# Kernel optimization log

Measured on AMD Instinct MI355X. Metric: run time of the kernel, lower is better.

The kernel has to match this reference:

```python
import jax, jax.numpy as jnp
import numpy as np

D = 256
N_EDGES = 8192
N_CORNERS = 4096


def setup_inputs() -> dict:
    key = jax.random.key(0)
    ks = jax.random.split(key, 8)
    scale = 1.0 / np.sqrt(D)
    return {
        "edge_pred": jax.random.uniform(ks[0], (N_EDGES,), dtype=jnp.float32),
        "edge_corner": jax.random.randint(ks[1], (N_EDGES, 2), 0, N_CORNERS, dtype=jnp.int64),
        "all_corners": jax.random.uniform(ks[2], (N_CORNERS, 2), dtype=jnp.float32),
        "edge_x": jax.random.normal(ks[3], (N_EDGES, D), dtype=jnp.float32),
        "image_x": jax.random.normal(ks[4], (1024,), dtype=jnp.float32),
        "W1": jax.random.normal(ks[5], (D, D), dtype=jnp.float32) * scale,
        "b1": jnp.zeros((D,), dtype=jnp.float32),
        "W2": jax.random.normal(ks[6], (D, D), dtype=jnp.float32) * scale,
        "b2": jnp.zeros((D,), dtype=jnp.float32),
        "W3": jax.random.normal(ks[7], (3 * D, D), dtype=jnp.float32) * scale,
        "b3": jnp.zeros((D,), dtype=jnp.float32),
    }


def _linear_block(x, W, b):
    # LinearBlock: Linear followed by ReLU
    return jax.nn.relu(x @ W + b)


def reference(edge_pred, edge_corner, all_corners, edge_x, image_x, W1, b1, W2, b2, W3, b3):
    # 'fully' branch of MPModule.forward. edge_pred/edge_corner/all_corners/image_x
    # are unused in this branch (kept for signature fidelity).
    e1 = _linear_block(edge_x, W1, b1)              # [N, D]
    # (e1.unsqueeze(1) * e1).mean(-1) == (e1 @ e1.T) / D   -> [N, N]
    sim1 = (e1 @ e1.T) / D
    e2 = _linear_block(edge_x, W2, b2)
    sim2 = (e2 @ e2.T) / D
    # (edge_x * sim.unsqueeze(-1)).sum(1) == sim @ edge_x  -> [N, D]
    agg1 = sim1 @ edge_x
    agg2 = sim2 @ edge_x
    cat = jnp.concatenate([edge_x, agg1, agg2], axis=-1)  # [N, 3D]
    out = _linear_block(cat, W3, b3)                      # [N, D]
    return out
```

## Files before the change

kernel.cpp:

```cpp
#include <hip/hip_runtime.h>

#define NE 8192
#define DD 256
#define NSPLIT 32

typedef __attribute__((ext_vector_type(8))) short short8;
typedef __attribute__((ext_vector_type(4))) short short4v;
typedef __attribute__((ext_vector_type(8))) __bf16 bf16x8;
typedef __attribute__((ext_vector_type(4))) float floatx4;

__device__ __forceinline__ unsigned short f2bf(float f) {
  union { float f; unsigned int i; } v; v.f = f;
  unsigned int r = v.i + 0x7fffu + ((v.i >> 16) & 1u);
  return (unsigned short)(r >> 16);
}

__device__ __forceinline__ floatx4 mfma_bf16(short8 a, short8 b, floatx4 c) {
  return __builtin_amdgcn_mfma_f32_16x16x32_bf16(
      __builtin_bit_cast(bf16x8, a), __builtin_bit_cast(bf16x8, b), c, 0, 0, 0);
}

__device__ __forceinline__ void tcvt_tile(const float* __restrict__ src, int C,
                                          unsigned short* __restrict__ dst, int R,
                                          int r0, int c0, int tid) {
  __shared__ float ls[64][68];
  const int rr = tid >> 4;
  const int c4 = (tid & 15) * 4;
#pragma unroll
  for (int k = 0; k < 4; ++k) {
    floatx4 v = *(const floatx4*)&src[(size_t)(r0 + rr + k * 16) * C + c0 + c4];
    *(floatx4*)&ls[rr + k * 16][c4] = v;
  }
  __syncthreads();
  const int cc = tid >> 2;
  const int rb = (tid & 3) * 16;
  short8 o0, o1;
#pragma unroll
  for (int i = 0; i < 8; ++i) {
    o0[i] = (short)f2bf(ls[rb + i][cc]);
    o1[i] = (short)f2bf(ls[rb + 8 + i][cc]);
  }
  unsigned short* dp = &dst[(size_t)(c0 + cc) * R + r0 + rb];
  *(short8*)dp = o0;
  *(short8*)(dp + 8) = o1;
}

__global__ void cvt_all(const float* __restrict__ x, unsigned short* __restrict__ xb,
                        unsigned short* __restrict__ xT,
                        const float* __restrict__ W1, unsigned short* __restrict__ W1t,
                        const float* __restrict__ W2, unsigned short* __restrict__ W2t,
                        const float* __restrict__ W3, unsigned short* __restrict__ W3t0) {
  const int b = blockIdx.x;
  const int tid = threadIdx.x;
  if (b < 1024) {
    int i = b * 256 + tid;
    floatx4 a = ((const floatx4*)x)[2 * i];
    floatx4 c = ((const floatx4*)x)[2 * i + 1];
    short8 o;
#pragma unroll
    for (int k = 0; k < 4; ++k) { o[k] = (short)f2bf(a[k]); o[4 + k] = (short)f2bf(c[k]); }
    ((short8*)xb)[i] = o;
  } else if (b < 1536) {
    int t = b - 1024;
    tcvt_tile(x, DD, xT, NE, (t >> 2) * 64, (t & 3) * 64, tid);
  } else if (b < 1552) {
    int t = b - 1536;
    tcvt_tile(W1, DD, W1t, DD, (t >> 2) * 64, (t & 3) * 64, tid);
  } else if (b < 1568) {
    int t = b - 1552;
    tcvt_tile(W2, DD, W2t, DD, (t >> 2) * 64, (t & 3) * 64, tid);
  } else {
    int t = b - 1568;
    tcvt_tile(W3, DD, W3t0, DD, (t >> 2) * 64, (t & 3) * 64, tid);
  }
}

template <bool F32OUT, bool STORE_T>
__global__ __launch_bounds__(256, 2)
void gemm_bias_relu(const unsigned short* __restrict__ A0, const unsigned short* __restrict__ B0,
                    const unsigned short* __restrict__ A1, const unsigned short* __restrict__ B1,
                    const unsigned short* __restrict__ A2, const unsigned short* __restrict__ B2,
                    int nseg, const float* __restrict__ bias, void* __restrict__ outp,
                    unsigned short* __restrict__ outT,
                    const unsigned short* __restrict__ B0alt, const float* __restrict__ biasalt,
                    void* __restrict__ outalt, unsigned short* __restrict__ outTalt)
{
  __shared__ unsigned short lds_a[128 * 40];
  __shared__ unsigned short lds_b[128 * 40];

  const unsigned short* B0s = B0;
  const float* bi = bias;
  void* op = outp;
  unsigned short* ot = outT;
  if (blockIdx.z) { B0s = B0alt; bi = biasalt; op = outalt; ot = outTalt; }

  const int tid  = threadIdx.x;
  const int lane = tid & 63;
  const int wave = tid >> 6;
  const int q = lane >> 4, r = lane & 15;
  const int wr = (wave >> 1) * 64;
  const int wc = (wave & 1) * 64;
  const int row0 = blockIdx.y * 128;
  const int col0 = blockIdx.x * 128;

  floatx4 acc[4][4];
#pragma unroll
  for (int i = 0; i < 4; ++i)
#pragma unroll
    for (int j = 0; j < 4; ++j) acc[i][j] = (floatx4){0.f, 0.f, 0.f, 0.f};

  const int sr = tid >> 1;
  const int sk = (tid & 1) * 16;

  for (int s = 0; s < nseg; ++s) {
    const unsigned short* A = (s == 0) ? A0 : ((s == 1) ? A1 : A2);
    const unsigned short* B = (s == 0) ? B0s : ((s == 1) ? B1 : B2);
    for (int kc = 0; kc < 256; kc += 32) {
      const unsigned short* ga = A + (size_t)(row0 + sr) * DD + kc + sk;
      short8 av0 = *(const short8*)ga;
      short8 av1 = *(const short8*)(ga + 8);
      const unsigned short* gb = B + (size_t)(col0 + sr) * DD + kc + sk;
      short8 bv0 = *(const short8*)gb;
      short8 bv1 = *(const short8*)(gb + 8);

      *(short8*)&lds_a[sr * 40 + sk]     = av0;
      *(short8*)&lds_a[sr * 40 + sk + 8] = av1;
      *(short8*)&lds_b[sr * 40 + sk]     = bv0;
      *(short8*)&lds_b[sr * 40 + sk + 8] = bv1;
      __syncthreads();

      short8 af[4], bfr[4];
#pragma unroll
      for (int i = 0; i < 4; ++i)
        af[i] = *(const short8*)&lds_a[(wr + i * 16 + r) * 40 + q * 8];
#pragma unroll
      for (int j = 0; j < 4; ++j)
        bfr[j] = *(const short8*)&lds_b[(wc + j * 16 + r) * 40 + q * 8];
#pragma unroll
      for (int i = 0; i < 4; ++i)
#pragma unroll
        for (int j = 0; j < 4; ++j)
          acc[i][j] = mfma_bf16(af[i], bfr[j], acc[i][j]);
      __syncthreads();
    }
  }

#pragma unroll
  for (int j = 0; j < 4; ++j) {
    const int col = col0 + wc + j * 16 + r;
    const float bv = bi[col];
#pragma unroll
    for (int i = 0; i < 4; ++i) {
      const int rowb = row0 + wr + i * 16 + q * 4;
      float v[4];
#pragma unroll
      for (int t = 0; t < 4; ++t) v[t] = fmaxf(acc[i][j][t] + bv, 0.0f);
      if (F32OUT) {
#pragma unroll
        for (int t = 0; t < 4; ++t)
          ((float*)op)[(size_t)(rowb + t) * DD + col] = v[t];
      } else {
#pragma unroll
        for (int t = 0; t < 4; ++t)
          ((unsigned short*)op)[(size_t)(rowb + t) * DD + col] = f2bf(v[t]);
      }
      if (STORE_T) {
        short4v tv;
#pragma unroll
        for (int t = 0; t < 4; ++t) tv[t] = (short)f2bf(v[t]);
        *(short4v*)&ot[(size_t)col * NE + rowb] = tv;
      }
    }
  }
}

__global__ __launch_bounds__(256, 2)
void atb_partial(const unsigned short* __restrict__ e1T,
                 const unsigned short* __restrict__ e2T,
                 const unsigned short* __restrict__ xT,
                 float* __restrict__ P_T)
{
  __shared__ unsigned short lds_e[128 * 40];
  __shared__ unsigned short lds_x[128 * 40];

  const int tid  = threadIdx.x;
  const int lane = tid & 63;
  const int wave = tid >> 6;
  const int q = lane >> 4, r = lane & 15;
  const int wr = (wave >> 1) * 64, wc = (wave & 1) * 64;
  const int m0 = (blockIdx.x >> 1) * 128;
  const int n0 = (blockIdx.x & 1) * 128;
  const int j0 = blockIdx.y * (NE / NSPLIT);
  const unsigned short* E = blockIdx.z ? e2T : e1T;
  float* P = P_T + (size_t)(blockIdx.z * NSPLIT + blockIdx.y) * 65536;

  floatx4 acc[4][4];
#pragma unroll
  for (int i = 0; i < 4; ++i)
#pragma unroll
    for (int j = 0; j < 4; ++j) acc[i][j] = (floatx4){0.f, 0.f, 0.f, 0.f};

  const int sr = tid >> 1;
  const int sk = (tid & 1) * 16;

  for (int jc = 0; jc < NE / NSPLIT; jc += 32) {
    const unsigned short* ge = E + (size_t)(m0 + sr) * NE + j0 + jc + sk;
    short8 ev0 = *(const short8*)ge;
    short8 ev1 = *(const short8*)(ge + 8);
    const unsigned short* gx = xT + (size_t)(n0 + sr) * NE + j0 + jc + sk;
    short8 xv0 = *(const short8*)gx;
    short8 xv1 = *(const short8*)(gx + 8);
    *(short8*)&lds_e[sr * 40 + sk]     = ev0;
    *(short8*)&lds_e[sr * 40 + sk + 8] = ev1;
    *(short8*)&lds_x[sr * 40 + sk]     = xv0;
    *(short8*)&lds_x[sr * 40 + sk + 8] = xv1;
    __syncthreads();

    short8 af[4], bfr[4];
#pragma unroll
    for (int i = 0; i < 4; ++i)
      af[i] = *(const short8*)&lds_e[(wr + i * 16 + r) * 40 + q * 8];
#pragma unroll
    for (int j = 0; j < 4; ++j)
      bfr[j] = *(const short8*)&lds_x[(wc + j * 16 + r) * 40 + q * 8];
#pragma unroll
    for (int i = 0; i < 4; ++i)
#pragma unroll
      for (int j = 0; j < 4; ++j)
        acc[i][j] = mfma_bf16(af[i], bfr[j], acc[i][j]);
    __syncthreads();
  }

#pragma unroll
  for (int i = 0; i < 4; ++i)
#pragma unroll
    for (int j = 0; j < 4; ++j) {
      const int n = n0 + wc + j * 16 + r;
      const int m = m0 + wr + i * 16 + q * 4;
      *(floatx4*)&P[(size_t)n * DD + m] = acc[i][j];
    }
}

__global__ void reduce_g(const float* __restrict__ P_T, float* __restrict__ G_T) {
  int idx = blockIdx.x * 256 + threadIdx.x;
  int z = idx >> 14;
  int off = idx & 16383;
  const floatx4* Pp = (const floatx4*)P_T;
  floatx4 s = (floatx4){0.f, 0.f, 0.f, 0.f};
#pragma unroll
  for (int y = 0; y < NSPLIT; ++y)
    s += Pp[(size_t)(z * NSPLIT + y) * 16384 + off];
  ((floatx4*)G_T)[idx] = s;
}

__global__ __launch_bounds__(256, 2)
void h_kernel(const float* __restrict__ G_T, const float* __restrict__ W3,
              unsigned short* __restrict__ H1t, unsigned short* __restrict__ H2t)
{
  __shared__ float lg[32 * 68];
  __shared__ float lw[32 * 68];
  const int z = blockIdx.z;
  const float* G = G_T + (size_t)z * 65536;
  unsigned short* Ht = z ? H2t : H1t;
  const float* Wb = W3 + (size_t)(256 + z * 256) * DD;
  const int k0 = blockIdx.y * 64;
  const int m0 = blockIdx.x * 64;
  const int tid = threadIdx.x;
  const int ty = tid >> 4, tx = tid & 15;

  float acc[4][4] = {};

  for (int lc = 0; lc < 256; lc += 32) {
    {
      int lr = tid >> 3;
      int e8 = (tid & 7) * 8;
      const float* gp = G + (size_t)(lc + lr) * DD + k0 + e8;
      *(floatx4*)&lg[lr * 68 + e8]     = *(const floatx4*)gp;
      *(floatx4*)&lg[lr * 68 + e8 + 4] = *(const floatx4*)(gp + 4);
      const float* wp = Wb + (size_t)(lc + lr) * DD + m0 + e8;
      *(floatx4*)&lw[lr * 68 + e8]     = *(const floatx4*)wp;
      *(floatx4*)&lw[lr * 68 + e8 + 4] = *(const floatx4*)(wp + 4);
    }
    __syncthreads();
#pragma unroll
    for (int l = 0; l < 32; ++l) {
      float a[4], b[4];
#pragma unroll
      for (int i = 0; i < 4; ++i) a[i] = lg[l * 68 + ty * 4 + i];
#pragma unroll
      for (int j = 0; j < 4; ++j) b[j] = lw[l * 68 + tx * 4 + j];
#pragma unroll
      for (int i = 0; i < 4; ++i)
#pragma unroll
        for (int j = 0; j < 4; ++j) acc[i][j] = fmaf(a[i], b[j], acc[i][j]);
    }
    __syncthreads();
  }
#pragma unroll
  for (int j = 0; j < 4; ++j) {
    short4v tv;
#pragma unroll
    for (int i = 0; i < 4; ++i) tv[i] = (short)f2bf(acc[i][j] * 0.00390625f);
    *(short4v*)&Ht[(size_t)(m0 + tx * 4 + j) * DD + k0 + ty * 4] = tv;
  }
}

extern "C" void kernel_launch(void* const* d_in, const int* in_sizes, int n_in,
                              void* d_out, int out_size, void* d_ws, size_t ws_size,
                              hipStream_t stream) {
  (void)in_sizes; (void)n_in; (void)out_size; (void)ws_size;
  const float* x   = (const float*)d_in[3];
  const float* W1  = (const float*)d_in[5];
  const float* b1  = (const float*)d_in[6];
  const float* W2  = (const float*)d_in[7];
  const float* b2  = (const float*)d_in[8];
  const float* W3  = (const float*)d_in[9];
  const float* b3  = (const float*)d_in[10];
  float* out = (float*)d_out;

  char* ws = (char*)d_ws;
  const size_t MB = 1u << 20;
  const size_t KB = 1u << 10;
  unsigned short* xb   = (unsigned short*)ws;
  unsigned short* xT   = (unsigned short*)(ws + 4 * MB);
  unsigned short* e1   = (unsigned short*)(ws + 8 * MB);
  unsigned short* e2   = (unsigned short*)(ws + 12 * MB);
  unsigned short* e1T  = (unsigned short*)(ws + 16 * MB);
  unsigned short* e2T  = (unsigned short*)(ws + 20 * MB);
  unsigned short* W1t  = (unsigned short*)(ws + 24 * MB);
  unsigned short* W2t  = (unsigned short*)(ws + 24 * MB + 128 * KB);
  unsigned short* W3t0 = (unsigned short*)(ws + 24 * MB + 256 * KB);
  unsigned short* H1t  = (unsigned short*)(ws + 24 * MB + 384 * KB);
  unsigned short* H2t  = (unsigned short*)(ws + 24 * MB + 512 * KB);
  float* G_T           = (float*)(ws + 24 * MB + 640 * KB);
  float* P_T           = (float*)(ws + 26 * MB);

  cvt_all<<<1584, 256, 0, stream>>>(x, xb, xT, W1, W1t, W2, W2t, W3, W3t0);

  gemm_bias_relu<false, true><<<dim3(2, 64, 2), 256, 0, stream>>>(
      xb, W1t, nullptr, nullptr, nullptr, nullptr, 1, b1, e1, e1T, W2t, b2, e2, e2T);

  atb_partial<<<dim3(4, NSPLIT, 2), 256, 0, stream>>>(e1T, e2T, xT, P_T);
  reduce_g<<<128, 256, 0, stream>>>(P_T, G_T);

  h_kernel<<<dim3(4, 4, 2), 256, 0, stream>>>(G_T, W3, H1t, H2t);

  gemm_bias_relu<true, false><<<dim3(2, 64, 1), 256, 0, stream>>>(
      xb, W3t0, e1, H1t, e2, H2t, 3, b3, out, nullptr, nullptr, nullptr, nullptr, nullptr);
}
```

Baseline: 144.7 us.

## Fuse all stages into one persistent kernel with software grid barriers

Replaces the six separate launches (convert, e1/e2 GEMM, partial A^T B, reduce, H GEMM, final GEMM) with one 256-block persistent kernel. The stages are separated by atomic-counter grid barriers, which removes launch gaps and inter-kernel idle time. The final GEMM is retiled to 64-row blocks so that all 256 blocks take part in it. The barrier scheme relies on all 256 blocks being co-resident. The reset uses a magic word that stays set across calls, so on repeated invocations later blocks may read stale counters before block 0 clears them, which risks a race.

```diff
diff --git a/kernel.cpp b/kernel.cpp
--- a/kernel.cpp
+++ b/kernel.cpp
@@ -3,6 +3,8 @@
 #define NE 8192
 #define DD 256
 #define NSPLIT 32
+#define NB 256
+#define MAGIC 0x13572468
 
 typedef __attribute__((ext_vector_type(8))) short short8;
 typedef __attribute__((ext_vector_type(4))) short short4v;
@@ -20,115 +22,131 @@
       __builtin_bit_cast(bf16x8, a), __builtin_bit_cast(bf16x8, b), c, 0, 0, 0);
 }
 
-__device__ __forceinline__ void tcvt_tile(const float* __restrict__ src, int C,
+__device__ __forceinline__ void grid_barrier(int* cnt) {
+  __syncthreads();
+  if (threadIdx.x == 0) {
+    __threadfence();
+    __hip_atomic_fetch_add(cnt, 1, __ATOMIC_ACQ_REL, __HIP_MEMORY_SCOPE_AGENT);
+    while (__hip_atomic_load(cnt, __ATOMIC_ACQUIRE, __HIP_MEMORY_SCOPE_AGENT) < NB)
+      __builtin_amdgcn_s_sleep(1);
+  }
+  __syncthreads();
+}
+
+__device__ __forceinline__ void tcvt_tile(float* lsf,
+                                          const float* __restrict__ src, int C,
                                           unsigned short* __restrict__ dst, int R,
                                           int r0, int c0, int tid) {
-  __shared__ float ls[64][68];
   const int rr = tid >> 4;
   const int c4 = (tid & 15) * 4;
 #pragma unroll
-  for (int k = 0; k < 4; ++k) {
-    floatx4 v = *(const floatx4*)&src[(size_t)(r0 + rr + k * 16) * C + c0 + c4];
-    *(floatx4*)&ls[rr + k * 16][c4] = v;
-  }
+  for (int k = 0; k < 4; ++k)
+    *(floatx4*)&lsf[(rr + k * 16) * 68 + c4] =
+        *(const floatx4*)&src[(size_t)(r0 + rr + k * 16) * C + c0 + c4];
   __syncthreads();
   const int cc = tid >> 2;
   const int rb = (tid & 3) * 16;
   short8 o0, o1;
 #pragma unroll
   for (int i = 0; i < 8; ++i) {
-    o0[i] = (short)f2bf(ls[rb + i][cc]);
-    o1[i] = (short)f2bf(ls[rb + 8 + i][cc]);
+    o0[i] = (short)f2bf(lsf[(rb + i) * 68 + cc]);
+    o1[i] = (short)f2bf(lsf[(rb + 8 + i) * 68 + cc]);
   }
   unsigned short* dp = &dst[(size_t)(c0 + cc) * R + r0 + rb];
   *(short8*)dp = o0;
   *(short8*)(dp + 8) = o1;
-}
-
-__global__ void cvt_all(const float* __restrict__ x, unsigned short* __restrict__ xb,
-                        unsigned short* __restrict__ xT,
-                        const float* __restrict__ W1, unsigned short* __restrict__ W1t,
-                        const float* __restrict__ W2, unsigned short* __restrict__ W2t,
-                        const float* __restrict__ W3, unsigned short* __restrict__ W3t0) {
-  const int b = blockIdx.x;
-  const int tid = threadIdx.x;
-  if (b < 1024) {
-    int i = b * 256 + tid;
+  __syncthreads();
+}
+
+__global__ __launch_bounds__(256, 2)
+void mp_mega(const float* __restrict__ x,
+             const float* __restrict__ W1, const float* __restrict__ b1,
+             const float* __restrict__ W2, const float* __restrict__ b2,
+             const float* __restrict__ W3, const float* __restrict__ b3,
+             float* __restrict__ out,
+             unsigned short* __restrict__ xb, unsigned short* __restrict__ xT,
+             unsigned short* __restrict__ e1, unsigned short* __restrict__ e2,
+             unsigned short* __restrict__ e1T, unsigned short* __restrict__ e2T,
+             unsigned short* __restrict__ W1t, unsigned short* __restrict__ W2t,
+             unsigned short* __restrict__ W3t0,
+             unsigned short* __restrict__ H1t, unsigned short* __restrict__ H2t,
+             float* __restrict__ G_T, float* __restrict__ P_T,
+             int* __restrict__ sync)
+{
+  __shared__ __align__(16) unsigned short sm[2 * 128 * 40];
+  unsigned short* lds_a = sm;
+  unsigned short* lds_b = sm + 128 * 40;
+  float* lsf = (float*)sm;
+
+  const int B = blockIdx.x;
+  const int T = threadIdx.x;
+  const int lane = T & 63;
+  const int wv = T >> 6;
+  const int q = lane >> 4, r = lane & 15;
+
+  if (B == 0 && T == 0) {
+    for (int i = 1; i <= 6; ++i)
+      __hip_atomic_store(&sync[i], 0, __ATOMIC_RELAXED, __HIP_MEMORY_SCOPE_AGENT);
+    __hip_atomic_store(&sync[0], MAGIC, __ATOMIC_RELEASE, __HIP_MEMORY_SCOPE_AGENT);
+  }
+  if (T == 0) {
+    while (__hip_atomic_load(&sync[0], __ATOMIC_ACQUIRE, __HIP_MEMORY_SCOPE_AGENT) != MAGIC)
+      __builtin_amdgcn_s_sleep(1);
+  }
+  __syncthreads();
+
+#pragma unroll
+  for (int p = 0; p < 4; ++p) {
+    int i = (p * NB + B) * 256 + T;
     floatx4 a = ((const floatx4*)x)[2 * i];
     floatx4 c = ((const floatx4*)x)[2 * i + 1];
     short8 o;
 #pragma unroll
     for (int k = 0; k < 4; ++k) { o[k] = (short)f2bf(a[k]); o[4 + k] = (short)f2bf(c[k]); }
     ((short8*)xb)[i] = o;
-  } else if (b < 1536) {
-    int t = b - 1024;
-    tcvt_tile(x, DD, xT, NE, (t >> 2) * 64, (t & 3) * 64, tid);
-  } else if (b < 1552) {
-    int t = b - 1536;
-    tcvt_tile(W1, DD, W1t, DD, (t >> 2) * 64, (t & 3) * 64, tid);
-  } else if (b < 1568) {
-    int t = b - 1552;
-    tcvt_tile(W2, DD, W2t, DD, (t >> 2) * 64, (t & 3) * 64, tid);
-  } else {
-    int t = b - 1568;
-    tcvt_tile(W3, DD, W3t0, DD, (t >> 2) * 64, (t & 3) * 64, tid);
-  }
-}
-
-template <bool F32OUT, bool STORE_T>
-__global__ __launch_bounds__(256, 2)
-void gemm_bias_relu(const unsigned short* __restrict__ A0, const unsigned short* __restrict__ B0,
-                    const unsigned short* __restrict__ A1, const unsigned short* __restrict__ B1,
-                    const unsigned short* __restrict__ A2, const unsigned short* __restrict__ B2,
-                    int nseg, const float* __restrict__ bias, void* __restrict__ outp,
-                    unsigned short* __restrict__ outT,
-                    const unsigned short* __restrict__ B0alt, const float* __restrict__ biasalt,
-                    void* __restrict__ outalt, unsigned short* __restrict__ outTalt)
-{
-  __shared__ unsigned short lds_a[128 * 40];
-  __shared__ unsigned short lds_b[128 * 40];
-
-  const unsigned short* B0s = B0;
-  const float* bi = bias;
-  void* op = outp;
-  unsigned short* ot = outT;
-  if (blockIdx.z) { B0s = B0alt; bi = biasalt; op = outalt; ot = outTalt; }
-
-  const int tid  = threadIdx.x;
-  const int lane = tid & 63;
-  const int wave = tid >> 6;
-  const int q = lane >> 4, r = lane & 15;
-  const int wr = (wave >> 1) * 64;
-  const int wc = (wave & 1) * 64;
-  const int row0 = blockIdx.y * 128;
-  const int col0 = blockIdx.x * 128;
-
-  floatx4 acc[4][4];
-#pragma unroll
-  for (int i = 0; i < 4; ++i)
-#pragma unroll
-    for (int j = 0; j < 4; ++j) acc[i][j] = (floatx4){0.f, 0.f, 0.f, 0.f};
-
-  const int sr = tid >> 1;
-  const int sk = (tid & 1) * 16;
-
-  for (int s = 0; s < nseg; ++s) {
-    const unsigned short* A = (s == 0) ? A0 : ((s == 1) ? A1 : A2);
-    const unsigned short* B = (s == 0) ? B0s : ((s == 1) ? B1 : B2);
+  }
+#pragma unroll
+  for (int tt = 0; tt < 2; ++tt) {
+    int t = B * 2 + tt;
+    tcvt_tile(lsf, x, DD, xT, NE, (t >> 2) * 64, (t & 3) * 64, T);
+  }
+  if (B < 48) {
+    int t = B & 15;
+    const float* src = (B < 16) ? W1 : ((B < 32) ? W2 : W3);
+    unsigned short* dst = (B < 16) ? W1t : ((B < 32) ? W2t : W3t0);
+    tcvt_tile(lsf, src, DD, dst, DD, (t >> 2) * 64, (t & 3) * 64, T);
+  }
+  grid_barrier(&sync[1]);
+
+  {
+    const int z = B >> 7, t = B & 127;
+    const int col0 = (t & 1) * 128, row0 = (t >> 1) * 128;
+    const unsigned short* Bop = z ? W2t : W1t;
+    const float* bi = z ? b2 : b1;
+    unsigned short* eo = z ? e2 : e1;
+    unsigned short* eoT = z ? e2T : e1T;
+    const int wr = (wv >> 1) * 64, wc = (wv & 1) * 64;
+
+    floatx4 acc[4][4];
+#pragma unroll
+    for (int i = 0; i < 4; ++i)
+#pragma unroll
+      for (int j = 0; j < 4; ++j) acc[i][j] = (floatx4){0.f, 0.f, 0.f, 0.f};
+
+    const int sr = T >> 1;
+    const int sk = (T & 1) * 16;
     for (int kc = 0; kc < 256; kc += 32) {
-      const unsigned short* ga = A + (size_t)(row0 + sr) * DD + kc + sk;
+      const unsigned short* ga = xb + (size_t)(row0 + sr) * DD + kc + sk;
       short8 av0 = *(const short8*)ga;
       short8 av1 = *(const short8*)(ga + 8);
-      const unsigned short* gb = B + (size_t)(col0 + sr) * DD + kc + sk;
+      const unsigned short* gb = Bop + (size_t)(col0 + sr) * DD + kc + sk;
       short8 bv0 = *(const short8*)gb;
       short8 bv1 = *(const short8*)(gb + 8);
-
-      *(short8*)&lds_a[sr * 40 + sk]     = av0;
+      *(short8*)&lds_a[sr * 40 + sk] = av0;
       *(short8*)&lds_a[sr * 40 + sk + 8] = av1;
-      *(short8*)&lds_b[sr * 40 + sk]     = bv0;
+      *(short8*)&lds_b[sr * 40 + sk] = bv0;
       *(short8*)&lds_b[sr * 40 + sk + 8] = bv1;
       __syncthreads();
-
       short8 af[4], bfr[4];
 #pragma unroll
       for (int i = 0; i < 4; ++i)
@@ -143,165 +161,191 @@
           acc[i][j] = mfma_bf16(af[i], bfr[j], acc[i][j]);
       __syncthreads();
     }
-  }
-
-#pragma unroll
-  for (int j = 0; j < 4; ++j) {
-    const int col = col0 + wc + j * 16 + r;
-    const float bv = bi[col];
-#pragma unroll
-    for (int i = 0; i < 4; ++i) {
-      const int rowb = row0 + wr + i * 16 + q * 4;
-      float v[4];
-#pragma unroll
-      for (int t = 0; t < 4; ++t) v[t] = fmaxf(acc[i][j][t] + bv, 0.0f);
-      if (F32OUT) {
-#pragma unroll
-        for (int t = 0; t < 4; ++t)
-          ((float*)op)[(size_t)(rowb + t) * DD + col] = v[t];
-      } else {
-#pragma unroll
-        for (int t = 0; t < 4; ++t)
-          ((unsigned short*)op)[(size_t)(rowb + t) * DD + col] = f2bf(v[t]);
-      }
-      if (STORE_T) {
+#pragma unroll
+    for (int j = 0; j < 4; ++j) {
+      const int col = col0 + wc + j * 16 + r;
+      const float bv = bi[col];
+#pragma unroll
+      for (int i = 0; i < 4; ++i) {
+        const int rowb = row0 + wr + i * 16 + q * 4;
+        float v[4];
         short4v tv;
 #pragma unroll
-        for (int t = 0; t < 4; ++t) tv[t] = (short)f2bf(v[t]);
-        *(short4v*)&ot[(size_t)col * NE + rowb] = tv;
-      }
-    }
-  }
-}
-
-__global__ __launch_bounds__(256, 2)
-void atb_partial(const unsigned short* __restrict__ e1T,
-                 const unsigned short* __restrict__ e2T,
-                 const unsigned short* __restrict__ xT,
-                 float* __restrict__ P_T)
-{
-  __shared__ unsigned short lds_e[128 * 40];
-  __shared__ unsigned short lds_x[128 * 40];
-
-  const int tid  = threadIdx.x;
-  const int lane = tid & 63;
-  const int wave = tid >> 6;
-  const int q = lane >> 4, r = lane & 15;
-  const int wr = (wave >> 1) * 64, wc = (wave & 1) * 64;
-  const int m0 = (blockIdx.x >> 1) * 128;
-  const int n0 = (blockIdx.x & 1) * 128;
-  const int j0 = blockIdx.y * (NE / NSPLIT);
-  const unsigned short* E = blockIdx.z ? e2T : e1T;
-  float* P = P_T + (size_t)(blockIdx.z * NSPLIT + blockIdx.y) * 65536;
-
-  floatx4 acc[4][4];
-#pragma unroll
-  for (int i = 0; i < 4; ++i)
-#pragma unroll
-    for (int j = 0; j < 4; ++j) acc[i][j] = (floatx4){0.f, 0.f, 0.f, 0.f};
-
-  const int sr = tid >> 1;
-  const int sk = (tid & 1) * 16;
-
-  for (int jc = 0; jc < NE / NSPLIT; jc += 32) {
-    const unsigned short* ge = E + (size_t)(m0 + sr) * NE + j0 + jc + sk;
-    short8 ev0 = *(const short8*)ge;
-    short8 ev1 = *(const short8*)(ge + 8);
-    const unsigned short* gx = xT + (size_t)(n0 + sr) * NE + j0 + jc + sk;
-    short8 xv0 = *(const short8*)gx;
-    short8 xv1 = *(const short8*)(gx + 8);
-    *(short8*)&lds_e[sr * 40 + sk]     = ev0;
-    *(short8*)&lds_e[sr * 40 + sk + 8] = ev1;
-    *(short8*)&lds_x[sr * 40 + sk]     = xv0;
-    *(short8*)&lds_x[sr * 40 + sk + 8] = xv1;
-    __syncthreads();
-
-    short8 af[4], bfr[4];
+        for (int t2 = 0; t2 < 4; ++t2) {
+          v[t2] = fmaxf(acc[i][j][t2] + bv, 0.0f);
+          unsigned short h = f2bf(v[t2]);
+          tv[t2] = (short)h;
+          eo[(size_t)(rowb + t2) * DD + col] = h;
+        }
+        *(short4v*)&eoT[(size_t)col * NE + rowb] = tv;
+      }
+    }
+  }
+  grid_barrier(&sync[2]);
+
+  {
+    const int z = B >> 7, rest = B & 127;
+    const int quad = rest & 3, split = rest >> 2;
+    const int m0 = (quad >> 1) * 128, n0 = (quad & 1) * 128;
+    const int j0 = split * (NE / NSPLIT);
+    const unsigned short* E = z ? e2T : e1T;
+    float* P = P_T + (size_t)(z * NSPLIT + split) * 65536;
+    const int wr = (wv >> 1) * 64, wc = (wv & 1) * 64;
+
+    floatx4 acc[4][4];
 #pragma unroll
     for (int i = 0; i < 4; ++i)
-      af[i] = *(const short8*)&lds_e[(wr + i * 16 + r) * 40 + q * 8];
-#pragma unroll
-    for (int j = 0; j < 4; ++j)
-      bfr[j] = *(const short8*)&lds_x[(wc + j * 16 + r) * 40 + q * 8];
+#pragma unroll
+      for (int j = 0; j < 4; ++j) acc[i][j] = (floatx4){0.f, 0.f, 0.f, 0.f};
+
+    const int sr = T >> 1;
+    const int sk = (T & 1) * 16;
+    for (int jc = 0; jc < NE / NSPLIT; jc += 32) {
+      const unsigned short* ge = E + (size_t)(m0 + sr) * NE + j0 + jc + sk;
+      short8 ev0 = *(const short8*)ge;
+      short8 ev1 = *(const short8*)(ge + 8);
+      const unsigned short* gx = xT + (size_t)(n0 + sr) * NE + j0 + jc + sk;
+      short8 xv0 = *(const short8*)gx;
+      short8 xv1 = *(const short8*)(gx + 8);
+      *(short8*)&lds_a[sr * 40 + sk] = ev0;
+      *(short8*)&lds_a[sr * 40 + sk + 8] = ev1;
+      *(short8*)&lds_b[sr * 40 + sk] = xv0;
+      *(short8*)&lds_b[sr * 40 + sk + 8] = xv1;
+      __syncthreads();
+      short8 af[4], bfr[4];
+#pragma unroll
+      for (int i = 0; i < 4; ++i)
+        af[i] = *(const short8*)&lds_a[(wr + i * 16 + r) * 40 + q * 8];
+#pragma unroll
+      for (int j = 0; j < 4; ++j)
+        bfr[j] = *(const short8*)&lds_b[(wc + j * 16 + r) * 40 + q * 8];
+#pragma unroll
+      for (int i = 0; i < 4; ++i)
+#pragma unroll
+        for (int j = 0; j < 4; ++j)
+          acc[i][j] = mfma_bf16(af[i], bfr[j], acc[i][j]);
+      __syncthreads();
+    }
 #pragma unroll
     for (int i = 0; i < 4; ++i)
 #pragma unroll
-      for (int j = 0; j < 4; ++j)
-        acc[i][j] = mfma_bf16(af[i], bfr[j], acc[i][j]);
-    __syncthreads();
-  }
-
-#pragma unroll
-  for (int i = 0; i < 4; ++i)
-#pragma unroll
-    for (int j = 0; j < 4; ++j) {
-      const int n = n0 + wc + j * 16 + r;
-      const int m = m0 + wr + i * 16 + q * 4;
-      *(floatx4*)&P[(size_t)n * DD + m] = acc[i][j];
-    }
-}
-
-__global__ void reduce_g(const float* __restrict__ P_T, float* __restrict__ G_T) {
-  int idx = blockIdx.x * 256 + threadIdx.x;
-  int z = idx >> 14;
-  int off = idx & 16383;
-  const floatx4* Pp = (const floatx4*)P_T;
-  floatx4 s = (floatx4){0.f, 0.f, 0.f, 0.f};
-#pragma unroll
-  for (int y = 0; y < NSPLIT; ++y)
-    s += Pp[(size_t)(z * NSPLIT + y) * 16384 + off];
-  ((floatx4*)G_T)[idx] = s;
-}
-
-__global__ __launch_bounds__(256, 2)
-void h_kernel(const float* __restrict__ G_T, const float* __restrict__ W3,
-              unsigned short* __restrict__ H1t, unsigned short* __restrict__ H2t)
-{
-  __shared__ float lg[32 * 68];
-  __shared__ float lw[32 * 68];
-  const int z = blockIdx.z;
-  const float* G = G_T + (size_t)z * 65536;
-  unsigned short* Ht = z ? H2t : H1t;
-  const float* Wb = W3 + (size_t)(256 + z * 256) * DD;
-  const int k0 = blockIdx.y * 64;
-  const int m0 = blockIdx.x * 64;
-  const int tid = threadIdx.x;
-  const int ty = tid >> 4, tx = tid & 15;
-
-  float acc[4][4] = {};
-
-  for (int lc = 0; lc < 256; lc += 32) {
-    {
-      int lr = tid >> 3;
-      int e8 = (tid & 7) * 8;
+      for (int j = 0; j < 4; ++j) {
+        const int n = n0 + wc + j * 16 + r;
+        const int m = m0 + wr + i * 16 + q * 4;
+        *(floatx4*)&P[(size_t)n * DD + m] = acc[i][j];
+      }
+  }
+  grid_barrier(&sync[3]);
+
+  if (T < 128) {
+    int idx = B * 128 + T;
+    int z = idx >> 14, off = idx & 16383;
+    const floatx4* Pp = (const floatx4*)P_T;
+    floatx4 s = (floatx4){0.f, 0.f, 0.f, 0.f};
+#pragma unroll
+    for (int y = 0; y < NSPLIT; ++y)
+      s += Pp[(size_t)(z * NSPLIT + y) * 16384 + off];
+    ((floatx4*)G_T)[idx] = s;
+  }
+  grid_barrier(&sync[4]);
+
+  if (B < 32) {
+    float* lg = (float*)sm;
+    float* lw = (float*)sm + 32 * 68;
+    const int z = B >> 4, rr = B & 15;
+    const int m0 = (rr & 3) * 64, k0 = (rr >> 2) * 64;
+    const float* G = G_T + (size_t)z * 65536;
+    unsigned short* Ht = z ? H2t : H1t;
+    const float* Wb = W3 + (size_t)(256 + z * 256) * DD;
+    const int ty = T >> 4, tx = T & 15;
+    float acc[4][4] = {};
+    for (int lc = 0; lc < 256; lc += 32) {
+      int lr = T >> 3;
+      int e8 = (T & 7) * 8;
       const float* gp = G + (size_t)(lc + lr) * DD + k0 + e8;
-      *(floatx4*)&lg[lr * 68 + e8]     = *(const floatx4*)gp;
+      *(floatx4*)&lg[lr * 68 + e8] = *(const floatx4*)gp;
       *(floatx4*)&lg[lr * 68 + e8 + 4] = *(const floatx4*)(gp + 4);
       const float* wp = Wb + (size_t)(lc + lr) * DD + m0 + e8;
-      *(floatx4*)&lw[lr * 68 + e8]     = *(const floatx4*)wp;
+      *(floatx4*)&lw[lr * 68 + e8] = *(const floatx4*)wp;
       *(floatx4*)&lw[lr * 68 + e8 + 4] = *(const floatx4*)(wp + 4);
-    }
-    __syncthreads();
-#pragma unroll
-    for (int l = 0; l < 32; ++l) {
-      float a[4], b[4];
-#pragma unroll
-      for (int i = 0; i < 4; ++i) a[i] = lg[l * 68 + ty * 4 + i];
-#pragma unroll
-      for (int j = 0; j < 4; ++j) b[j] = lw[l * 68 + tx * 4 + j];
-#pragma unroll
-      for (int i = 0; i < 4; ++i)
-#pragma unroll
-        for (int j = 0; j < 4; ++j) acc[i][j] = fmaf(a[i], b[j], acc[i][j]);
-    }
-    __syncthreads();
-  }
-#pragma unroll
-  for (int j = 0; j < 4; ++j) {
-    short4v tv;
-#pragma unroll
-    for (int i = 0; i < 4; ++i) tv[i] = (short)f2bf(acc[i][j] * 0.00390625f);
-    *(short4v*)&Ht[(size_t)(m0 + tx * 4 + j) * DD + k0 + ty * 4] = tv;
+      __syncthreads();
+#pragma unroll
+      for (int l = 0; l < 32; ++l) {
+        float a[4], b[4];
+#pragma unroll
+        for (int i = 0; i < 4; ++i) a[i] = lg[l * 68 + ty * 4 + i];
+#pragma unroll
+        for (int j = 0; j < 4; ++j) b[j] = lw[l * 68 + tx * 4 + j];
+#pragma unroll
+        for (int i = 0; i < 4; ++i)
+#pragma unroll
+          for (int j = 0; j < 4; ++j) acc[i][j] = fmaf(a[i], b[j], acc[i][j]);
+      }
+      __syncthreads();
+    }
+#pragma unroll
+    for (int j = 0; j < 4; ++j) {
+      short4v tv;
+#pragma unroll
+      for (int i = 0; i < 4; ++i) tv[i] = (short)f2bf(acc[i][j] * 0.00390625f);
+      *(short4v*)&Ht[(size_t)(m0 + tx * 4 + j) * DD + k0 + ty * 4] = tv;
+    }
+  }
+  grid_barrier(&sync[5]);
+
+  {
+    const int col0 = (B & 1) * 128;
+    const int row0 = (B >> 1) * 64;
+    const unsigned short* As[3] = {xb, e1, e2};
+    const unsigned short* Bs[3] = {W3t0, H1t, H2t};
+
+    floatx4 acc[4][2];
+#pragma unroll
+    for (int i = 0; i < 4; ++i)
+#pragma unroll
+      for (int j = 0; j < 2; ++j) acc[i][j] = (floatx4){0.f, 0.f, 0.f, 0.f};
+
+    const int arow = T >> 2, ak8 = (T & 3) * 8;
+    const int bn = T >> 1, bk16 = (T & 1) * 16;
+    for (int s = 0; s < 3; ++s) {
+      const unsigned short* A = As[s];
+      const unsigned short* Bo = Bs[s];
+      for (int kc = 0; kc < 256; kc += 32) {
+        short8 av = *(const short8*)(A + (size_t)(row0 + arow) * DD + kc + ak8);
+        const unsigned short* gb = Bo + (size_t)(col0 + bn) * DD + kc + bk16;
+        short8 bv0 = *(const short8*)gb;
+        short8 bv1 = *(const short8*)(gb + 8);
+        *(short8*)&lds_a[arow * 40 + ak8] = av;
+        *(short8*)&lds_b[bn * 40 + bk16] = bv0;
+        *(short8*)&lds_b[bn * 40 + bk16 + 8] = bv1;
+        __syncthreads();
+        short8 af[4], bfr[2];
+#pragma unroll
+        for (int i = 0; i < 4; ++i)
+          af[i] = *(const short8*)&lds_a[(i * 16 + r) * 40 + q * 8];
+#pragma unroll
+        for (int j = 0; j < 2; ++j)
+          bfr[j] = *(const short8*)&lds_b[(wv * 32 + j * 16 + r) * 40 + q * 8];
+#pragma unroll
+        for (int i = 0; i < 4; ++i)
+#pragma unroll
+          for (int j = 0; j < 2; ++j)
+            acc[i][j] = mfma_bf16(af[i], bfr[j], acc[i][j]);
+        __syncthreads();
+      }
+    }
+#pragma unroll
+    for (int j = 0; j < 2; ++j) {
+      const int col = col0 + wv * 32 + j * 16 + r;
+      const float bv = b3[col];
+#pragma unroll
+      for (int i = 0; i < 4; ++i) {
+        const int rowb = row0 + i * 16 + q * 4;
+#pragma unroll
+        for (int t2 = 0; t2 < 4; ++t2)
+          out[(size_t)(rowb + t2) * DD + col] = fmaxf(acc[i][j][t2] + bv, 0.0f);
+      }
+    }
   }
 }
 
@@ -309,13 +353,13 @@
                               void* d_out, int out_size, void* d_ws, size_t ws_size,
                               hipStream_t stream) {
   (void)in_sizes; (void)n_in; (void)out_size; (void)ws_size;
-  const float* x   = (const float*)d_in[3];
-  const float* W1  = (const float*)d_in[5];
-  const float* b1  = (const float*)d_in[6];
-  const float* W2  = (const float*)d_in[7];
-  const float* b2  = (const float*)d_in[8];
-  const float* W3  = (const float*)d_in[9];
-  const float* b3  = (const float*)d_in[10];
+  const float* x  = (const float*)d_in[3];
+  const float* W1 = (const float*)d_in[5];
+  const float* b1 = (const float*)d_in[6];
+  const float* W2 = (const float*)d_in[7];
+  const float* b2 = (const float*)d_in[8];
+  const float* W3 = (const float*)d_in[9];
+  const float* b3 = (const float*)d_in[10];
   float* out = (float*)d_out;
 
   char* ws = (char*)d_ws;
@@ -334,17 +378,9 @@
   unsigned short* H2t  = (unsigned short*)(ws + 24 * MB + 512 * KB);
   float* G_T           = (float*)(ws + 24 * MB + 640 * KB);
   float* P_T           = (float*)(ws + 26 * MB);
-
-  cvt_all<<<1584, 256, 0, stream>>>(x, xb, xT, W1, W1t, W2, W2t, W3, W3t0);
-
-  gemm_bias_relu<false, true><<<dim3(2, 64, 2), 256, 0, stream>>>(
-      xb, W1t, nullptr, nullptr, nullptr, nullptr, 1, b1, e1, e1T, W2t, b2, e2, e2T);
-
-  atb_partial<<<dim3(4, NSPLIT, 2), 256, 0, stream>>>(e1T, e2T, xT, P_T);
-  reduce_g<<<128, 256, 0, stream>>>(P_T, G_T);
-
-  h_kernel<<<dim3(4, 4, 2), 256, 0, stream>>>(G_T, W3, H1t, H2t);
-
-  gemm_bias_relu<true, false><<<dim3(2, 64, 1), 256, 0, stream>>>(
-      xb, W3t0, e1, H1t, e2, H2t, 3, b3, out, nullptr, nullptr, nullptr, nullptr, nullptr);
-}
+  int* sync            = (int*)(ws + 48 * MB);
+
+  mp_mega<<<NB, 256, 0, stream>>>(x, W1, b1, W2, b2, W3, b3, out,
+                                  xb, xT, e1, e2, e1T, e2T,
+                                  W1t, W2t, W3t0, H1t, H2t, G_T, P_T, sync);
+}
```

Result: slower. 305.4 us (+111.1%).
